# Optimization experiments

Hardware: AMD Instinct MI355X
Metric: run time of the kernel (lower is better)

The kernel has to match this reference:

```python
import jax, jax.numpy as jnp
import numpy as np

# Dims: CrossMambaBlock(dim=256, H=32, W=32); inner Mamba(d_model=512, expand=1,
# d_state=16, bimamba_type='v2', if_devide_out=True, use_norm=True)
B, N, C = 4, 1024, 256
D_MODEL = 2 * C          # 512 (mamba d_model)
D_INNER = D_MODEL        # expand=1
D_STATE = 16
DT_RANK = 32             # ceil(512/16)
D_CONV = 4


def _ln(x, g, b, eps=1e-5):
    m = jnp.mean(x, axis=-1, keepdims=True)
    v = jnp.var(x, axis=-1, keepdims=True)
    return (x - m) * jax.lax.rsqrt(v + eps) * g + b


def _depthwise_causal_conv(x, w, b):
    # x: (B, d, L), w: (d, 1, k) -> causal conv (pad k-1 left), matches Conv1d(padding=k-1)[..., :L]
    y = jax.lax.conv_general_dilated(
        x, w, window_strides=(1,), padding=[(D_CONV - 1, 0)],
        feature_group_count=D_INNER, dimension_numbers=('NCH', 'OIH', 'NCH'))
    return y + b[None, :, None]


def _selective_scan(u, delta, A, Bm, Cm, Dv):
    # u, delta: (B, d, L); A: (d, n); Bm, Cm: (B, n, L); Dv: (d,)
    dA = jnp.exp(jnp.einsum('bdl,dn->lbdn', delta, A))
    dBu = jnp.einsum('bdl,bnl->lbdn', delta * u, Bm)
    Ct = jnp.transpose(Cm, (2, 0, 1))  # (L, B, n)

    def step(h, inp):
        dA_t, dBu_t, c_t = inp
        h = dA_t * h + dBu_t                          # (B, d, n)
        y = jnp.einsum('bdn,bn->bd', h, c_t)
        return h, y

    h0 = jnp.zeros((u.shape[0], u.shape[1], A.shape[1]), u.dtype)
    _, ys = jax.lax.scan(step, h0, (dA, dBu, Ct))
    y = jnp.transpose(ys, (1, 2, 0))                  # (B, d, L)
    return y + Dv[:, None] * u


def _mamba_dir(xz, conv_w, conv_b, xproj_w, dt_w, dt_b, A_log, Dv):
    x, z = jnp.split(xz, 2, axis=1)                   # each (B, d_inner, L)
    x = jax.nn.silu(_depthwise_causal_conv(x, conv_w, conv_b))
    x_dbl = jnp.einsum('bdl,ed->bel', x, xproj_w)     # (B, dt_rank+2n, L)
    dt = x_dbl[:, :DT_RANK]
    Bm = x_dbl[:, DT_RANK:DT_RANK + D_STATE]
    Cm = x_dbl[:, DT_RANK + D_STATE:]
    delta = jax.nn.softplus(jnp.einsum('brl,dr->bdl', dt, dt_w) + dt_b[None, :, None])
    A = -jnp.exp(A_log)
    y = _selective_scan(x, delta, A, Bm, Cm, Dv)
    return y * jax.nn.silu(z)                         # (B, d_inner, L)


def _forward(input0, input1, norm0_g, norm0_b, norm1_g, norm1_b, in_proj_w,
             convf_w, convf_b, convb_w, convb_b, xprojf_w, xprojb_w,
             dtf_w, dtf_b, dtb_w, dtb_b, A_log_f, A_log_b, D_f, D_b,
             mnorm_g, mnorm_b, outproj_w, pnorm_g, pnorm_b,
             projback_w, projback_b, cw_w, cw_b, cwln_g, cwln_b):
    i0 = jnp.nan_to_num(input0, nan=0.0, posinf=1.0, neginf=-1.0)
    i1 = jnp.nan_to_num(input1, nan=0.0, posinf=1.0, neginf=-1.0)
    skip = i0
    x0n = _ln(i0, norm0_g, norm0_b)
    x1n = _ln(i1, norm1_g, norm1_b)
    combined = jnp.concatenate([x0n, x1n], axis=-1)   # (B, N, 2C)
    weight = jax.nn.sigmoid(_ln(combined @ cw_w.T + cw_b, cwln_g, cwln_b))
    weight = jnp.clip(weight, 0.01, 0.99)
    # Mamba (bimamba v2): shared in_proj, two directional scans
    xz = jnp.einsum('bld,ed->bel', combined, in_proj_w)  # (B, 2*d_inner, L)
    out_f = _mamba_dir(xz, convf_w, convf_b, xprojf_w, dtf_w, dtf_b, A_log_f, D_f)
    out_b = _mamba_dir(jnp.flip(xz, -1), convb_w, convb_b, xprojb_w, dtb_w, dtb_b, A_log_b, D_b)
    y = (out_f + jnp.flip(out_b, -1)) * 0.5           # if_devide_out
    y = _ln(jnp.transpose(y, (0, 2, 1)), mnorm_g, mnorm_b)  # use_norm
    out = y @ outproj_w.T                              # (B, N, 2C)
    out = _ln(out, pnorm_g, pnorm_b)
    out = out @ projback_w.T + projback_b              # (B, N, C)
    out = jnp.nan_to_num(out, nan=0.0, posinf=1.0, neginf=-1.0)
    out = out * weight + x0n * (1.0 - weight)
    return out + skip


def setup_inputs() -> dict:
    key = jax.random.key(0)
    ks = iter(jax.random.split(key, 40))
    def rn(shape, s=0.02):
        return jax.random.normal(next(ks), shape, jnp.float32) * s
    inp = {}
    inp['input0'] = jax.random.normal(next(ks), (B, N, C), jnp.float32)
    inp['input1'] = jax.random.normal(next(ks), (B, N, C), jnp.float32)
    for nm in ['norm0', 'norm1']:
        inp[nm + '_g'] = jnp.ones((C,), jnp.float32)
        inp[nm + '_b'] = jnp.zeros((C,), jnp.float32)
    inp['in_proj_w'] = rn((2 * D_INNER, D_MODEL))
    for t in ['f', 'b']:
        inp['conv%s_w' % t] = rn((D_INNER, 1, D_CONV), 0.1)
        inp['conv%s_b' % t] = jnp.zeros((D_INNER,), jnp.float32)
        inp['xproj%s_w' % t] = rn((DT_RANK + 2 * D_STATE, D_INNER))
        inp['dt%s_w' % t] = rn((D_INNER, DT_RANK), 0.05)
        inp['dt%s_b' % t] = rn((D_INNER,), 0.05)
        inp['A_log_%s' % t] = jnp.log(jnp.broadcast_to(
            jnp.arange(1, D_STATE + 1, dtype=jnp.float32), (D_INNER, D_STATE)))
        inp['D_%s' % t] = jnp.ones((D_INNER,), jnp.float32)
    inp['mnorm_g'] = jnp.ones((D_INNER,), jnp.float32)
    inp['mnorm_b'] = jnp.zeros((D_INNER,), jnp.float32)
    inp['outproj_w'] = rn((D_MODEL, D_INNER))
    inp['pnorm_g'] = jnp.ones((D_MODEL,), jnp.float32)
    inp['pnorm_b'] = jnp.zeros((D_MODEL,), jnp.float32)
    inp['projback_w'] = rn((C, D_MODEL))
    inp['projback_b'] = jnp.zeros((C,), jnp.float32)
    inp['cw_w'] = rn((C, D_MODEL))
    inp['cw_b'] = jnp.zeros((C,), jnp.float32)
    inp['cwln_g'] = jnp.ones((C,), jnp.float32)
    inp['cwln_b'] = jnp.zeros((C,), jnp.float32)
    return inp


def reference(input0, input1, norm0_g, norm0_b, norm1_g, norm1_b, in_proj_w,
              convf_w, convf_b, convb_w, convb_b, xprojf_w, xprojb_w,
              dtf_w, dtf_b, dtb_w, dtb_b, A_log_f, A_log_b, D_f, D_b,
              mnorm_g, mnorm_b, outproj_w, pnorm_g, pnorm_b,
              projback_w, projback_b, cw_w, cw_b, cwln_g, cwln_b):
    return _forward(input0, input1, norm0_g, norm0_b, norm1_g, norm1_b, in_proj_w,
                    convf_w, convf_b, convb_w, convb_b, xprojf_w, xprojb_w,
                    dtf_w, dtf_b, dtb_w, dtb_b, A_log_f, A_log_b, D_f, D_b,
                    mnorm_g, mnorm_b, outproj_w, pnorm_g, pnorm_b,
                    projback_w, projback_b, cw_w, cw_b, cwln_g, cwln_b)
```

## Files before the change

### kernel.cpp

```cpp
#include <hip/hip_runtime.h>

#define BDIM 4
#define SEQ 1024
#define CH 256
#define DMODEL 512
#define DINNER 512
#define DSTATE 16
#define DTRANK 32
#define NROWS (BDIM * SEQ)
#define NCHUNK 32
#define CHUNK (SEQ / NCHUNK)

typedef unsigned short ushort_t;

__device__ __forceinline__ float nan2num(float x) {
    if (isnan(x)) return 0.f;
    if (isinf(x)) return x > 0.f ? 1.f : -1.f;
    return x;
}

__device__ __forceinline__ float silu_f(float x) { return x / (1.f + __expf(-x)); }
__device__ __forceinline__ float sigmoid_f(float x) { return 1.f / (1.f + __expf(-x)); }
__device__ __forceinline__ float softplus_f(float x) {
    return x > 20.f ? x : log1pf(__expf(x));
}

__device__ __forceinline__ ushort_t f2bf(float x) {
    union { float f; unsigned u; } v; v.f = x;
    unsigned r = v.u + 0x7fff + ((v.u >> 16) & 1);
    return (ushort_t)(r >> 16);
}
__device__ __forceinline__ float bf2f(ushort_t x) {
    union { unsigned u; float f; } v; v.u = ((unsigned)x) << 16;
    return v.f;
}

using bf16x8 = __attribute__((ext_vector_type(8))) __bf16;
using f32x4  = __attribute__((ext_vector_type(4))) float;

__device__ __forceinline__ void wave_reduce2(float& s, float& q) {
#pragma unroll
    for (int m = 32; m > 0; m >>= 1) {
        s += __shfl_xor(s, m);
        q += __shfl_xor(q, m);
    }
}

#define SZ_INPROJ (1024 * 512)
#define SZ_CW     (256 * 512)
#define SZ_XP     (64 * 512)
#define SZ_DT     (512 * 32)
#define SZ_OUTP   (512 * 512)
#define SZ_PROJB  (256 * 512)
#define SZ_WTOT   (SZ_INPROJ + SZ_CW + 2 * SZ_XP + 2 * SZ_DT + SZ_OUTP + SZ_PROJB)

__global__ __launch_bounds__(256) void convert_weights_kernel(
        const float* __restrict__ w0, const float* __restrict__ w1,
        const float* __restrict__ w2, const float* __restrict__ w3,
        const float* __restrict__ w4, const float* __restrict__ w5,
        const float* __restrict__ w6, const float* __restrict__ w7,
        ushort_t* __restrict__ out) {
    int i = blockIdx.x * 256 + threadIdx.x;
    if (i >= SZ_WTOT) return;
    int j = i;
    const float* src;
    if (j < SZ_INPROJ) { src = w0; }
    else { j -= SZ_INPROJ;
        if (j < SZ_CW) { src = w1; }
        else { j -= SZ_CW;
            if (j < SZ_XP) { src = w2; }
            else { j -= SZ_XP;
                if (j < SZ_XP) { src = w3; }
                else { j -= SZ_XP;
                    if (j < SZ_DT) { src = w4; }
                    else { j -= SZ_DT;
                        if (j < SZ_DT) { src = w5; }
                        else { j -= SZ_DT;
                            if (j < SZ_OUTP) { src = w6; }
                            else { j -= SZ_OUTP; src = w7; }
                        }
                    }
                }
            }
        }
    }
    out[i] = f2bf(src[j]);
}

__global__ __launch_bounds__(256) void ln01_kernel(
        const float* __restrict__ i0, const float* __restrict__ i1,
        const float* __restrict__ g0, const float* __restrict__ b0,
        const float* __restrict__ g1, const float* __restrict__ b1,
        float* __restrict__ x0n, ushort_t* __restrict__ combined) {
    int w = threadIdx.x >> 6, lane = threadIdx.x & 63;
    int row = blockIdx.x * 4 + w;

    float4 v = ((const float4*)(i0 + row * CH))[lane];
    v.x = nan2num(v.x); v.y = nan2num(v.y); v.z = nan2num(v.z); v.w = nan2num(v.w);
    float s = v.x + v.y + v.z + v.w;
    float q = v.x * v.x + v.y * v.y + v.z * v.z + v.w * v.w;
    wave_reduce2(s, q);
    float m = s / (float)CH;
    float r = rsqrtf(q / (float)CH - m * m + 1e-5f);
    float4 g = ((const float4*)g0)[lane];
    float4 bb = ((const float4*)b0)[lane];
    float4 o;
    o.x = (v.x - m) * r * g.x + bb.x;
    o.y = (v.y - m) * r * g.y + bb.y;
    o.z = (v.z - m) * r * g.z + bb.z;
    o.w = (v.w - m) * r * g.w + bb.w;
    ((float4*)(x0n + row * CH))[lane] = o;
    *(ushort4*)(combined + row * DMODEL + lane * 4) =
        make_ushort4(f2bf(o.x), f2bf(o.y), f2bf(o.z), f2bf(o.w));

    v = ((const float4*)(i1 + row * CH))[lane];
    v.x = nan2num(v.x); v.y = nan2num(v.y); v.z = nan2num(v.z); v.w = nan2num(v.w);
    s = v.x + v.y + v.z + v.w;
    q = v.x * v.x + v.y * v.y + v.z * v.z + v.w * v.w;
    wave_reduce2(s, q);
    m = s / (float)CH;
    r = rsqrtf(q / (float)CH - m * m + 1e-5f);
    g = ((const float4*)g1)[lane];
    bb = ((const float4*)b1)[lane];
    o.x = (v.x - m) * r * g.x + bb.x;
    o.y = (v.y - m) * r * g.y + bb.y;
    o.z = (v.z - m) * r * g.z + bb.z;
    o.w = (v.w - m) * r * g.w + bb.w;
    *(ushort4*)(combined + row * DMODEL + CH + lane * 4) =
        make_ushort4(f2bf(o.x), f2bf(o.y), f2bf(o.z), f2bf(o.w));
}

template<int ACT>
__global__ __launch_bounds__(256) void gemm64_kernel(
        const ushort_t* __restrict__ A0, const ushort_t* __restrict__ A1, int lda,
        const ushort_t* __restrict__ W0, const ushort_t* __restrict__ W1, int ldw,
        ushort_t* __restrict__ C0, ushort_t* __restrict__ C1, int ldc,
        int K, const float* __restrict__ bias0, const float* __restrict__ bias1) {
    const ushort_t* A = blockIdx.z ? A1 : A0;
    const ushort_t* W = blockIdx.z ? W1 : W0;
    ushort_t* C = blockIdx.z ? C1 : C0;
    const float* bias = blockIdx.z ? bias1 : bias0;

    __shared__ __align__(16) ushort_t As[64][40];
    __shared__ __align__(16) ushort_t Ws[64][40];
    const int t = threadIdx.x;
    const int m0 = blockIdx.y * 64;
    const int n0 = blockIdx.x * 64;
    const int w = t >> 6;
    const int lane = t & 63;
    const int lane16 = lane & 15;
    const int quad = lane >> 4;
    const int wr = (w >> 1) * 32;
    const int wc = (w & 1) * 32;
    const int srow = t >> 2;
    const int sc8 = (t & 3) * 8;

    f32x4 acc[2][2] = {};

    for (int k0 = 0; k0 < K; k0 += 32) {
        float4 av = *(const float4*)(A + (m0 + srow) * lda + k0 + sc8);
        float4 wv = *(const float4*)(W + (n0 + srow) * ldw + k0 + sc8);
        *(float4*)&As[srow][sc8] = av;
        *(float4*)&Ws[srow][sc8] = wv;
        __syncthreads();

        bf16x8 af[2], bfr[2];
#pragma unroll
        for (int i = 0; i < 2; ++i) {
            af[i]  = *(bf16x8*)&As[wr + i * 16 + lane16][quad * 8];
            bfr[i] = *(bf16x8*)&Ws[wc + i * 16 + lane16][quad * 8];
        }
#pragma unroll
        for (int i = 0; i < 2; ++i)
#pragma unroll
            for (int j = 0; j < 2; ++j)
                acc[i][j] = __builtin_amdgcn_mfma_f32_16x16x32_bf16(af[i], bfr[j], acc[i][j], 0, 0, 0);
        __syncthreads();
    }

#pragma unroll
    for (int j = 0; j < 2; ++j) {
        int col = n0 + wc + j * 16 + lane16;
        float bv = bias ? bias[col] : 0.f;
#pragma unroll
        for (int i = 0; i < 2; ++i) {
#pragma unroll
            for (int r = 0; r < 4; ++r) {
                int row = m0 + wr + i * 16 + quad * 4 + r;
                float c = acc[i][j][r] + bv;
                if (ACT == 1) c = softplus_f(c);
                C[row * ldc + col] = f2bf(c);
            }
        }
    }
}

template<int ACT>
__global__ __launch_bounds__(256) void gemm128_kernel(
        const ushort_t* __restrict__ A0, const ushort_t* __restrict__ A1, int lda,
        const ushort_t* __restrict__ W0, const ushort_t* __restrict__ W1, int ldw,
        ushort_t* __restrict__ C0, ushort_t* __restrict__ C1, int ldc,
        int K, const float* __restrict__ bias0, const float* __restrict__ bias1) {
    const ushort_t* A = blockIdx.z ? A1 : A0;
    const ushort_t* W = blockIdx.z ? W1 : W0;
    ushort_t* C = blockIdx.z ? C1 : C0;
    const float* bias = blockIdx.z ? bias1 : bias0;

    __shared__ __align__(16) ushort_t As[128][40];
    __shared__ __align__(16) ushort_t Ws[64][40];
    const int t = threadIdx.x;
    const int m0 = blockIdx.y * 128;
    const int n0 = blockIdx.x * 64;
    const int w = t >> 6;
    const int lane = t & 63;
    const int lane16 = lane & 15;
    const int quad = lane >> 4;
    const int wr = (w >> 1) * 64;
    const int wc = (w & 1) * 32;
    const int arow = t >> 1;
    const int ac = (t & 1) * 16;
    const int srow = t >> 2;
    const int sc8 = (t & 3) * 8;

    f32x4 acc[4][2] = {};

    for (int k0 = 0; k0 < K; k0 += 32) {
        float4 a0 = *(const float4*)(A + (m0 + arow) * lda + k0 + ac);
        float4 a1 = *(const float4*)(A + (m0 + arow) * lda + k0 + ac + 8);
        float4 wv = *(const float4*)(W + (n0 + srow) * ldw + k0 + sc8);
        *(float4*)&As[arow][ac] = a0;
        *(float4*)&As[arow][ac + 8] = a1;
        *(float4*)&Ws[srow][sc8] = wv;
        __syncthreads();

        bf16x8 af[4], bfr[2];
#pragma unroll
        for (int i = 0; i < 4; ++i)
            af[i] = *(bf16x8*)&As[wr + i * 16 + lane16][quad * 8];
#pragma unroll
        for (int j = 0; j < 2; ++j)
            bfr[j] = *(bf16x8*)&Ws[wc + j * 16 + lane16][quad * 8];
#pragma unroll
        for (int i = 0; i < 4; ++i)
#pragma unroll
            for (int j = 0; j < 2; ++j)
                acc[i][j] = __builtin_amdgcn_mfma_f32_16x16x32_bf16(af[i], bfr[j], acc[i][j], 0, 0, 0);
        __syncthreads();
    }

#pragma unroll
    for (int j = 0; j < 2; ++j) {
        int col = n0 + wc + j * 16 + lane16;
        float bv = bias ? bias[col] : 0.f;
#pragma unroll
        for (int i = 0; i < 4; ++i) {
#pragma unroll
            for (int r = 0; r < 4; ++r) {
                int row = m0 + wr + i * 16 + quad * 4 + r;
                float c = acc[i][j][r] + bv;
                if (ACT == 1) c = softplus_f(c);
                C[row * ldc + col] = f2bf(c);
            }
        }
    }
}

__global__ __launch_bounds__(256) void gemm_projback_final_kernel(
        const ushort_t* __restrict__ A, int lda,
        const ushort_t* __restrict__ W, int ldw,
        int K, const float* __restrict__ bias,
        const ushort_t* __restrict__ wgt, const float* __restrict__ x0n,
        const float* __restrict__ i0, float* __restrict__ out) {
    __shared__ __align__(16) ushort_t As[64][40];
    __shared__ __align__(16) ushort_t Ws[64][40];
    const int t = threadIdx.x;
    const int m0 = blockIdx.y * 64;
    const int n0 = blockIdx.x * 64;
    const int w = t >> 6;
    const int lane = t & 63;
    const int lane16 = lane & 15;
    const int quad = lane >> 4;
    const int wr = (w >> 1) * 32;
    const int wc = (w & 1) * 32;
    const int srow = t >> 2;
    const int sc8 = (t & 3) * 8;

    f32x4 acc[2][2] = {};

    for (int k0 = 0; k0 < K; k0 += 32) {
        float4 av = *(const float4*)(A + (m0 + srow) * lda + k0 + sc8);
        float4 wv = *(const float4*)(W + (n0 + srow) * ldw + k0 + sc8);
        *(float4*)&As[srow][sc8] = av;
        *(float4*)&Ws[srow][sc8] = wv;
        __syncthreads();

        bf16x8 af[2], bfr[2];
#pragma unroll
        for (int i = 0; i < 2; ++i) {
            af[i]  = *(bf16x8*)&As[wr + i * 16 + lane16][quad * 8];
            bfr[i] = *(bf16x8*)&Ws[wc + i * 16 + lane16][quad * 8];
        }
#pragma unroll
        for (int i = 0; i < 2; ++i)
#pragma unroll
            for (int j = 0; j < 2; ++j)
                acc[i][j] = __builtin_amdgcn_mfma_f32_16x16x32_bf16(af[i], bfr[j], acc[i][j], 0, 0, 0);
        __syncthreads();
    }

#pragma unroll
    for (int j = 0; j < 2; ++j) {
        int col = n0 + wc + j * 16 + lane16;
        float bv = bias[col];
#pragma unroll
        for (int i = 0; i < 2; ++i) {
#pragma unroll
            for (int r = 0; r < 4; ++r) {
                int row = m0 + wr + i * 16 + quad * 4 + r;
                float o = nan2num(acc[i][j][r] + bv);
                float wv = bf2f(wgt[row * CH + col]);
                float xv = x0n[row * CH + col];
                float sk = nan2num(i0[row * CH + col]);
                out[row * CH + col] = o * wv + xv * (1.f - wv) + sk;
            }
        }
    }
}

__global__ __launch_bounds__(256) void weight_ln_kernel(
        ushort_t* __restrict__ wbuf, const float* __restrict__ g, const float* __restrict__ b) {
    int w = threadIdx.x >> 6, lane = threadIdx.x & 63;
    int row = blockIdx.x * 4 + w;
    ushort4 raw = *(const ushort4*)(wbuf + row * CH + lane * 4);
    float4 v = make_float4(bf2f(raw.x), bf2f(raw.y), bf2f(raw.z), bf2f(raw.w));
    float s = v.x + v.y + v.z + v.w;
    float q = v.x * v.x + v.y * v.y + v.z * v.z + v.w * v.w;
    wave_reduce2(s, q);
    float m = s / (float)CH;
    float r = rsqrtf(q / (float)CH - m * m + 1e-5f);
    float4 g4 = ((const float4*)g)[lane];
    float4 b4 = ((const float4*)b)[lane];
    float ox = fminf(fmaxf(sigmoid_f((v.x - m) * r * g4.x + b4.x), 0.01f), 0.99f);
    float oy = fminf(fmaxf(sigmoid_f((v.y - m) * r * g4.y + b4.y), 0.01f), 0.99f);
    float oz = fminf(fmaxf(sigmoid_f((v.z - m) * r * g4.z + b4.z), 0.01f), 0.99f);
    float ow = fminf(fmaxf(sigmoid_f((v.w - m) * r * g4.w + b4.w), 0.01f), 0.99f);
    *(ushort4*)(wbuf + row * CH + lane * 4) = make_ushort4(f2bf(ox), f2bf(oy), f2bf(oz), f2bf(ow));
}

__global__ __launch_bounds__(256) void conv_both_kernel(
        const ushort_t* __restrict__ xz,
        const float* __restrict__ wf, const float* __restrict__ wbf,
        const float* __restrict__ wb, const float* __restrict__ wbb,
        ushort_t* __restrict__ outf, ushort_t* __restrict__ outb) {
    int flat = blockIdx.x * 256 + threadIdx.x;
    int d = flat & (DINNER - 1);
    int row = flat >> 9;
    int l = row & (SEQ - 1);
    int b = row >> 10;
    float accf = wbf[d], accb = wbb[d];
#pragma unroll
    for (int k = 0; k < 4; ++k) {
        int jf = l - 3 + k;
        if (jf >= 0) accf += bf2f(xz[(b * SEQ + jf) * (2 * DINNER) + d]) * wf[d * 4 + k];
        int jb = l + 3 - k;
        if (jb < SEQ) accb += bf2f(xz[(b * SEQ + jb) * (2 * DINNER) + d]) * wb[d * 4 + k];
    }
    outf[flat] = f2bf(silu_f(accf));
    outb[(b * SEQ + (SEQ - 1 - l)) * DINNER + d] = f2bf(silu_f(accb));
}

__global__ __launch_bounds__(256) void scan_pass1_kernel(
        const ushort_t* __restrict__ df, const ushort_t* __restrict__ db,
        const ushort_t* __restrict__ uf, const ushort_t* __restrict__ ub,
        const ushort_t* __restrict__ xf, const ushort_t* __restrict__ xb,
        const float* __restrict__ Alf, const float* __restrict__ Alb,
        float* __restrict__ cAf, float* __restrict__ cAb,
        float* __restrict__ cHf, float* __restrict__ cHb) {
    const int dir = blockIdx.z >> 2;
    const int b = blockIdx.z & 3;
    const ushort_t* delta = dir ? db : df;
    const ushort_t* u     = dir ? ub : uf;
    const ushort_t* xdbl  = dir ? xb : xf;
    const float* A_log    = dir ? Alb : Alf;
    float* chunkA = dir ? cAb : cAf;
    float* chunkH = dir ? cHb : cHf;

    const int c = blockIdx.y;
    const int d = blockIdx.x * 256 + threadIdx.x;
    const int base = b * SEQ + c * CHUNK;

    __shared__ float sB[CHUNK][16];
    {
        int t = threadIdx.x;
        if (t < CHUNK * 2) {
            int row = t >> 1, f8 = (t & 1) * 8;
            float4 raw = *(const float4*)(xdbl + (base + row) * 64 + DTRANK + f8);
            const ushort_t* us = (const ushort_t*)&raw;
#pragma unroll
            for (int k = 0; k < 8; ++k) sB[row][f8 + k] = bf2f(us[k]);
        }
    }
    __syncthreads();

    float a[DSTATE];
#pragma unroll
    for (int n = 0; n < DSTATE; n += 4) {
        float4 al = *(const float4*)(A_log + d * DSTATE + n);
        a[n] = -__expf(al.x); a[n + 1] = -__expf(al.y);
        a[n + 2] = -__expf(al.z); a[n + 3] = -__expf(al.w);
    }
    float h[DSTATE];
#pragma unroll
    for (int n = 0; n < DSTATE; ++n) h[n] = 0.f;

    float sumdl = 0.f;
    float dl = bf2f(delta[base * DINNER + d]);
    float ul = bf2f(u[base * DINNER + d]);
    for (int s = 0; s < CHUNK; ++s) {
        int nrow = base + ((s + 1 < CHUNK) ? s + 1 : s);
        float dln = bf2f(delta[nrow * DINNER + d]);
        float uln = bf2f(u[nrow * DINNER + d]);
        float dlul = dl * ul;
        sumdl += dl;
#pragma unroll
        for (int g = 0; g < 4; ++g) {
            float4 B4 = *(const float4*)&sB[s][g * 4];
            float dA0 = __expf(dl * a[g * 4 + 0]);
            float dA1 = __expf(dl * a[g * 4 + 1]);
            float dA2 = __expf(dl * a[g * 4 + 2]);
            float dA3 = __expf(dl * a[g * 4 + 3]);
            h[g * 4 + 0] = dA0 * h[g * 4 + 0] + dlul * B4.x;
            h[g * 4 + 1] = dA1 * h[g * 4 + 1] + dlul * B4.y;
            h[g * 4 + 2] = dA2 * h[g * 4 + 2] + dlul * B4.z;
            h[g * 4 + 3] = dA3 * h[g * 4 + 3] + dlul * B4.w;
        }
        dl = dln; ul = uln;
    }

    int idx = ((b * NCHUNK + c) * DINNER + d) * DSTATE;
#pragma unroll
    for (int n = 0; n < DSTATE; n += 4) {
        float4 P4 = make_float4(__expf(a[n] * sumdl), __expf(a[n + 1] * sumdl),
                                __expf(a[n + 2] * sumdl), __expf(a[n + 3] * sumdl));
        *(float4*)(chunkA + idx + n) = P4;
        *(float4*)(chunkH + idx + n) = make_float4(h[n], h[n + 1], h[n + 2], h[n + 3]);
    }
}

__global__ __launch_bounds__(256) void scan_pass2_kernel(
        const float* __restrict__ cAf, const float* __restrict__ cAb,
        float* __restrict__ cHf, float* __restrict__ cHb) {
    int tid = blockIdx.x * 256 + threadIdx.x;
    int dir = tid >> 15;
    int rr = tid & 32767;
    int b = rr >> 13;
    int rem = rr & 8191;
    const float* chunkA = dir ? cAb : cAf;
    float* chunkH = dir ? cHb : cHf;
    float h = 0.f;
    for (int c = 0; c < NCHUNK; ++c) {
        int idx = (b * NCHUNK + c) * (DINNER * DSTATE) + rem;
        float Ac = chunkA[idx];
        float Hc = chunkH[idx];
        chunkH[idx] = h;
        h = Ac * h + Hc;
    }
}

__global__ __launch_bounds__(256) void scan_pass3_kernel(
        const ushort_t* __restrict__ df, const ushort_t* __restrict__ db,
        const ushort_t* __restrict__ uf, const ushort_t* __restrict__ ub,
        const ushort_t* __restrict__ xf, const ushort_t* __restrict__ xb,
        const float* __restrict__ Alf, const float* __restrict__ Alb,
        const float* __restrict__ Dvf, const float* __restrict__ Dvb,
        const float* __restrict__ hfb, const float* __restrict__ hbb,
        ushort_t* __restrict__ yfo, ushort_t* __restrict__ ybo) {
    const int dir = blockIdx.z >> 2;
    const int b = blockIdx.z & 3;
    const ushort_t* delta = dir ? db : df;
    const ushort_t* u     = dir ? ub : uf;
    const ushort_t* xdbl  = dir ? xb : xf;
    const float* A_log    = dir ? Alb : Alf;
    const float* Dv       = dir ? Dvb : Dvf;
    const float* hin      = dir ? hbb : hfb;
    ushort_t* yout        = dir ? ybo : yfo;

    const int c = blockIdx.y;
    const int d = blockIdx.x * 256 + threadIdx.x;
    const int base = b * SEQ + c * CHUNK;

    __shared__ float sBC[CHUNK][32];
    {
        int t = threadIdx.x;
        if (t < CHUNK * 4) {
            int row = t >> 2, f8 = (t & 3) * 8;
            float4 raw = *(const float4*)(xdbl + (base + row) * 64 + DTRANK + f8);
            const ushort_t* us = (const ushort_t*)&raw;
#pragma unroll
            for (int k = 0; k < 8; ++k) sBC[row][f8 + k] = bf2f(us[k]);
        }
    }
    __syncthreads();

    float a[DSTATE];
#pragma unroll
    for (int n = 0; n < DSTATE; n += 4) {
        float4 al = *(const float4*)(A_log + d * DSTATE + n);
        a[n] = -__expf(al.x); a[n + 1] = -__expf(al.y);
        a[n + 2] = -__expf(al.z); a[n + 3] = -__expf(al.w);
    }
    float h[DSTATE];
    {
        int idx = ((b * NCHUNK + c) * DINNER + d) * DSTATE;
#pragma unroll
        for (int n = 0; n < DSTATE; n += 4) {
            float4 h4 = *(const float4*)(hin + idx + n);
            h[n] = h4.x; h[n + 1] = h4.y; h[n + 2] = h4.z; h[n + 3] = h4.w;
        }
    }
    const float Dd = Dv[d];

    float dl = bf2f(delta[base * DINNER + d]);
    float ul = bf2f(u[base * DINNER + d]);
    for (int s = 0; s < CHUNK; ++s) {
        int nrow = base + ((s + 1 < CHUNK) ? s + 1 : s);
        float dln = bf2f(delta[nrow * DINNER + d]);
        float uln = bf2f(u[nrow * DINNER + d]);
        float dlul = dl * ul;
        float y = 0.f;
#pragma unroll
        for (int g = 0; g < 4; ++g) {
            float4 B4 = *(const float4*)&sBC[s][g * 4];
            float4 C4 = *(const float4*)&sBC[s][16 + g * 4];
            float dA0 = __expf(dl * a[g * 4 + 0]);
            float dA1 = __expf(dl * a[g * 4 + 1]);
            float dA2 = __expf(dl * a[g * 4 + 2]);
            float dA3 = __expf(dl * a[g * 4 + 3]);
            h[g * 4 + 0] = dA0 * h[g * 4 + 0] + dlul * B4.x;
            h[g * 4 + 1] = dA1 * h[g * 4 + 1] + dlul * B4.y;
            h[g * 4 + 2] = dA2 * h[g * 4 + 2] + dlul * B4.z;
            h[g * 4 + 3] = dA3 * h[g * 4 + 3] + dlul * B4.w;
            y += h[g * 4 + 0] * C4.x + h[g * 4 + 1] * C4.y
               + h[g * 4 + 2] * C4.z + h[g * 4 + 3] * C4.w;
        }
        int lpos = c * CHUNK + s;
        int orow = b * SEQ + (dir ? (SEQ - 1 - lpos) : lpos);
        yout[orow * DINNER + d] = f2bf(y + Dd * ul);
        dl = dln; ul = uln;
    }
}

__global__ __launch_bounds__(256) void combine_mnorm_kernel(
        const ushort_t* __restrict__ yf, const ushort_t* __restrict__ yb,
        const ushort_t* __restrict__ xz,
        const float* __restrict__ g, const float* __restrict__ b,
        ushort_t* __restrict__ yn) {
    int w = threadIdx.x >> 6, lane = threadIdx.x & 63;
    int row = blockIdx.x * 4 + w;
    float4 rf = *(const float4*)(yf + row * DINNER + lane * 8);
    float4 rb = *(const float4*)(yb + row * DINNER + lane * 8);
    float4 rz = *(const float4*)(xz + row * (2 * DINNER) + DINNER + lane * 8);
    const ushort_t* uf = (const ushort_t*)&rf;
    const ushort_t* ub = (const ushort_t*)&rb;
    const ushort_t* uz = (const ushort_t*)&rz;
    float v[8];
    float s = 0.f, q = 0.f;
#pragma unroll
    for (int k = 0; k < 8; ++k) {
        float val = 0.5f * (bf2f(uf[k]) + bf2f(ub[k])) * silu_f(bf2f(uz[k]));
        v[k] = val; s += val; q += val * val;
    }
    wave_reduce2(s, q);
    float m = s / (float)DINNER;
    float r = rsqrtf(q / (float)DINNER - m * m + 1e-5f);
    ushort_t o[8];
#pragma unroll
    for (int k = 0; k < 8; ++k)
        o[k] = f2bf((v[k] - m) * r * g[lane * 8 + k] + b[lane * 8 + k]);
    *(ushort4*)(yn + row * DINNER + lane * 8) = make_ushort4(o[0], o[1], o[2], o[3]);
    *(ushort4*)(yn + row * DINNER + lane * 8 + 4) = make_ushort4(o[4], o[5], o[6], o[7]);
}

__global__ __launch_bounds__(256) void ln512_kernel(
        const ushort_t* __restrict__ in,
        const float* __restrict__ g, const float* __restrict__ b,
        ushort_t* __restrict__ out) {
    int w = threadIdx.x >> 6, lane = threadIdx.x & 63;
    int row = blockIdx.x * 4 + w;
    float4 raw = *(const float4*)(in + row * DMODEL + lane * 8);
    const ushort_t* us = (const ushort_t*)&raw;
    float v[8];
    float s = 0.f, q = 0.f;
#pragma unroll
    for (int k = 0; k < 8; ++k) {
        v[k] = bf2f(us[k]); s += v[k]; q += v[k] * v[k];
    }
    wave_reduce2(s, q);
    float m = s / (float)DMODEL;
    float r = rsqrtf(q / (float)DMODEL - m * m + 1e-5f);
    ushort_t o[8];
#pragma unroll
    for (int k = 0; k < 8; ++k)
        o[k] = f2bf((v[k] - m) * r * g[lane * 8 + k] + b[lane * 8 + k]);
    *(ushort4*)(out + row * DMODEL + lane * 8) = make_ushort4(o[0], o[1], o[2], o[3]);
    *(ushort4*)(out + row * DMODEL + lane * 8 + 4) = make_ushort4(o[4], o[5], o[6], o[7]);
}

extern "C" void kernel_launch(void* const* d_in, const int* in_sizes, int n_in,
                              void* d_out, int out_size, void* d_ws, size_t ws_size,
                              hipStream_t stream) {
    (void)in_sizes; (void)n_in; (void)out_size; (void)ws_size;
    const float* input0    = (const float*)d_in[0];
    const float* input1    = (const float*)d_in[1];
    const float* norm0_g   = (const float*)d_in[2];
    const float* norm0_b   = (const float*)d_in[3];
    const float* norm1_g   = (const float*)d_in[4];
    const float* norm1_b   = (const float*)d_in[5];
    const float* in_proj_w = (const float*)d_in[6];
    const float* convf_w   = (const float*)d_in[7];
    const float* convf_b   = (const float*)d_in[8];
    const float* xprojf_w  = (const float*)d_in[9];
    const float* dtf_w     = (const float*)d_in[10];
    const float* dtf_b     = (const float*)d_in[11];
    const float* A_log_f   = (const float*)d_in[12];
    const float* D_f       = (const float*)d_in[13];
    const float* convb_w   = (const float*)d_in[14];
    const float* convb_b   = (const float*)d_in[15];
    const float* xprojb_w  = (const float*)d_in[16];
    const float* dtb_w     = (const float*)d_in[17];
    const float* dtb_b     = (const float*)d_in[18];
    const float* A_log_b   = (const float*)d_in[19];
    const float* D_b       = (const float*)d_in[20];
    const float* mnorm_g   = (const float*)d_in[21];
    const float* mnorm_b   = (const float*)d_in[22];
    const float* outproj_w = (const float*)d_in[23];
    const float* pnorm_g   = (const float*)d_in[24];
    const float* pnorm_b   = (const float*)d_in[25];
    const float* projback_w= (const float*)d_in[26];
    const float* projback_b= (const float*)d_in[27];
    const float* cw_w      = (const float*)d_in[28];
    const float* cw_b      = (const float*)d_in[29];
    const float* cwln_g    = (const float*)d_in[30];
    const float* cwln_b    = (const float*)d_in[31];

    float* wsf = (float*)d_ws;
    float* x0n      = wsf;
    float* chunkA_f = x0n + 1048576;
    float* chunkA_b = chunkA_f + 1048576;
    float* chunkH_f = chunkA_b + 1048576;
    float* chunkH_b = chunkH_f + 1048576;
    ushort_t* wsu = (ushort_t*)(chunkH_b + 1048576);
    ushort_t* combined = wsu;
    ushort_t* xz       = combined + 2097152;
    ushort_t* weight   = xz + 4194304;
    ushort_t* xdbl_f   = weight + 1048576;
    ushort_t* xdbl_b   = xdbl_f + 262144;
    ushort_t* xconv_f  = xdbl_b + 262144;
    ushort_t* xconv_b  = xconv_f + 2097152;
    ushort_t* delta_f  = xconv_b + 2097152;
    ushort_t* delta_b  = delta_f + 2097152;
    ushort_t* y_f      = delta_b + 2097152;
    ushort_t* y_b      = y_f + 2097152;
    ushort_t* yn       = y_b + 2097152;
    ushort_t* o1       = yn + 2097152;
    ushort_t* on1      = o1 + 2097152;
    ushort_t* wb       = on1 + 2097152;
    ushort_t* w_inproj = wb;
    ushort_t* w_cw     = w_inproj + SZ_INPROJ;
    ushort_t* w_xpf    = w_cw + SZ_CW;
    ushort_t* w_xpb    = w_xpf + SZ_XP;
    ushort_t* w_dtf    = w_xpb + SZ_XP;
    ushort_t* w_dtb    = w_dtf + SZ_DT;
    ushort_t* w_outp   = w_dtb + SZ_DT;
    ushort_t* w_projb  = w_outp + SZ_OUTP;

    convert_weights_kernel<<<(SZ_WTOT + 255) / 256, 256, 0, stream>>>(
        in_proj_w, cw_w, xprojf_w, xprojb_w, dtf_w, dtb_w, outproj_w, projback_w, wb);

    ln01_kernel<<<NROWS / 4, 256, 0, stream>>>(input0, input1, norm0_g, norm0_b,
                                               norm1_g, norm1_b, x0n, combined);

    gemm128_kernel<0><<<dim3(16, 32, 1), 256, 0, stream>>>(
        combined, combined, DMODEL, w_inproj, w_inproj, DMODEL,
        xz, xz, 2 * DINNER, DMODEL, nullptr, nullptr);

    gemm64_kernel<0><<<dim3(4, 64, 1), 256, 0, stream>>>(
        combined, combined, DMODEL, w_cw, w_cw, DMODEL,
        weight, weight, CH, DMODEL, cw_b, cw_b);

    weight_ln_kernel<<<NROWS / 4, 256, 0, stream>>>(weight, cwln_g, cwln_b);

    conv_both_kernel<<<NROWS * DINNER / 256, 256, 0, stream>>>(
        xz, convf_w, convf_b, convb_w, convb_b, xconv_f, xconv_b);

    gemm64_kernel<0><<<dim3(1, 64, 2), 256, 0, stream>>>(
        xconv_f, xconv_b, DINNER, w_xpf, w_xpb, DINNER,
        xdbl_f, xdbl_b, 64, DINNER, nullptr, nullptr);

    gemm128_kernel<1><<<dim3(8, 32, 2), 256, 0, stream>>>(
        xdbl_f, xdbl_b, 64, w_dtf, w_dtb, DTRANK,
        delta_f, delta_b, DINNER, DTRANK, dtf_b, dtb_b);

    dim3 sgrid(DINNER / 256, NCHUNK, 2 * BDIM);
    scan_pass1_kernel<<<sgrid, 256, 0, stream>>>(
        delta_f, delta_b, xconv_f, xconv_b, xdbl_f, xdbl_b, A_log_f, A_log_b,
        chunkA_f, chunkA_b, chunkH_f, chunkH_b);
    scan_pass2_kernel<<<256, 256, 0, stream>>>(chunkA_f, chunkA_b, chunkH_f, chunkH_b);
    scan_pass3_kernel<<<sgrid, 256, 0, stream>>>(
        delta_f, delta_b, xconv_f, xconv_b, xdbl_f, xdbl_b, A_log_f, A_log_b,
        D_f, D_b, chunkH_f, chunkH_b, y_f, y_b);

    combine_mnorm_kernel<<<NROWS / 4, 256, 0, stream>>>(y_f, y_b, xz, mnorm_g, mnorm_b, yn);

    gemm128_kernel<0><<<dim3(8, 32, 1), 256, 0, stream>>>(
        yn, yn, DINNER, w_outp, w_outp, DINNER,
        o1, o1, DMODEL, DINNER, nullptr, nullptr);

    ln512_kernel<<<NROWS / 4, 256, 0, stream>>>(o1, pnorm_g, pnorm_b, on1);

    gemm_projback_final_kernel<<<dim3(4, 64, 1), 256, 0, stream>>>(
        on1, DMODEL, w_projb, DMODEL, DMODEL, projback_b,
        weight, x0n, input0, (float*)d_out);
}
```

Before: 276.5 us.

## Fuse scan output pass with gate and norm, vectorize conv, use more chunks

The final scan pass now handles both directions for a chunk in one 512-thread block. It pairs forward chunk c with the matching reversed backward chunk, so it can average the two outputs, apply the SiLU(z) gate and the per-row LayerNorm in registers and shared memory. This removes the separate combine_mnorm kernel and the y_f/y_b intermediate buffers. The depthwise conv kernel is rewritten so each thread processes 8 channels with 16-byte vector loads and stores, reusing a 7-row window for both directions. The chunk count doubles to 64 for more scan parallelism, which costs larger chunk-state buffers and more work in the cross-chunk pass. The register prefetch in pass1 is also dropped.

```diff
diff --git a/kernel.cpp b/kernel.cpp
--- a/kernel.cpp
+++ b/kernel.cpp
@@ -8,7 +8,7 @@
 #define DSTATE 16
 #define DTRANK 32
 #define NROWS (BDIM * SEQ)
-#define NCHUNK 32
+#define NCHUNK 64
 #define CHUNK (SEQ / NCHUNK)
 
 typedef unsigned short ushort_t;
@@ -352,21 +352,58 @@
         const float* __restrict__ wf, const float* __restrict__ wbf,
         const float* __restrict__ wb, const float* __restrict__ wbb,
         ushort_t* __restrict__ outf, ushort_t* __restrict__ outb) {
-    int flat = blockIdx.x * 256 + threadIdx.x;
-    int d = flat & (DINNER - 1);
-    int row = flat >> 9;
-    int l = row & (SEQ - 1);
-    int b = row >> 10;
-    float accf = wbf[d], accb = wbb[d];
-#pragma unroll
-    for (int k = 0; k < 4; ++k) {
-        int jf = l - 3 + k;
-        if (jf >= 0) accf += bf2f(xz[(b * SEQ + jf) * (2 * DINNER) + d]) * wf[d * 4 + k];
-        int jb = l + 3 - k;
-        if (jb < SEQ) accb += bf2f(xz[(b * SEQ + jb) * (2 * DINNER) + d]) * wb[d * 4 + k];
-    }
-    outf[flat] = f2bf(silu_f(accf));
-    outb[(b * SEQ + (SEQ - 1 - l)) * DINNER + d] = f2bf(silu_f(accb));
+    const int t = threadIdx.x;
+    const int lane = t & 63;
+    const int row = blockIdx.x * 4 + (t >> 6);
+    const int l = row & (SEQ - 1);
+    const int b = row >> 10;
+    const int d0 = lane * 8;
+
+    float x[7][8];
+#pragma unroll
+    for (int j = 0; j < 7; ++j) {
+        int ll = l - 3 + j;
+        if (ll >= 0 && ll < SEQ) {
+            float4 raw = *(const float4*)(xz + (b * SEQ + ll) * (2 * DINNER) + d0);
+            const ushort_t* us = (const ushort_t*)&raw;
+#pragma unroll
+            for (int k = 0; k < 8; ++k) x[j][k] = bf2f(us[k]);
+        } else {
+#pragma unroll
+            for (int k = 0; k < 8; ++k) x[j][k] = 0.f;
+        }
+    }
+
+    float wfv[32], wbv[32];
+#pragma unroll
+    for (int q = 0; q < 8; ++q) {
+        float4 a = *(const float4*)(wf + d0 * 4 + q * 4);
+        wfv[q * 4] = a.x; wfv[q * 4 + 1] = a.y; wfv[q * 4 + 2] = a.z; wfv[q * 4 + 3] = a.w;
+        float4 c = *(const float4*)(wb + d0 * 4 + q * 4);
+        wbv[q * 4] = c.x; wbv[q * 4 + 1] = c.y; wbv[q * 4 + 2] = c.z; wbv[q * 4 + 3] = c.w;
+    }
+    float4 bf0 = *(const float4*)(wbf + d0), bf1 = *(const float4*)(wbf + d0 + 4);
+    float4 bb0 = *(const float4*)(wbb + d0), bb1 = *(const float4*)(wbb + d0 + 4);
+    float biasf[8] = {bf0.x, bf0.y, bf0.z, bf0.w, bf1.x, bf1.y, bf1.z, bf1.w};
+    float biasb[8] = {bb0.x, bb0.y, bb0.z, bb0.w, bb1.x, bb1.y, bb1.z, bb1.w};
+
+    ushort_t of[8], ob[8];
+#pragma unroll
+    for (int q = 0; q < 8; ++q) {
+        float accf = biasf[q], accb = biasb[q];
+#pragma unroll
+        for (int k = 0; k < 4; ++k) {
+            accf += x[k][q] * wfv[q * 4 + k];
+            accb += x[6 - k][q] * wbv[q * 4 + k];
+        }
+        of[q] = f2bf(silu_f(accf));
+        ob[q] = f2bf(silu_f(accb));
+    }
+    *(ushort4*)(outf + row * DINNER + d0)     = make_ushort4(of[0], of[1], of[2], of[3]);
+    *(ushort4*)(outf + row * DINNER + d0 + 4) = make_ushort4(of[4], of[5], of[6], of[7]);
+    ushort_t* pb = outb + (b * SEQ + (SEQ - 1 - l)) * DINNER + d0;
+    *(ushort4*)pb       = make_ushort4(ob[0], ob[1], ob[2], ob[3]);
+    *(ushort4*)(pb + 4) = make_ushort4(ob[4], ob[5], ob[6], ob[7]);
 }
 
 __global__ __launch_bounds__(256) void scan_pass1_kernel(
@@ -414,12 +451,10 @@
     for (int n = 0; n < DSTATE; ++n) h[n] = 0.f;
 
     float sumdl = 0.f;
-    float dl = bf2f(delta[base * DINNER + d]);
-    float ul = bf2f(u[base * DINNER + d]);
     for (int s = 0; s < CHUNK; ++s) {
-        int nrow = base + ((s + 1 < CHUNK) ? s + 1 : s);
-        float dln = bf2f(delta[nrow * DINNER + d]);
-        float uln = bf2f(u[nrow * DINNER + d]);
+        int row = base + s;
+        float dl = bf2f(delta[row * DINNER + d]);
+        float ul = bf2f(u[row * DINNER + d]);
         float dlul = dl * ul;
         sumdl += dl;
 #pragma unroll
@@ -434,7 +469,6 @@
             h[g * 4 + 2] = dA2 * h[g * 4 + 2] + dlul * B4.z;
             h[g * 4 + 3] = dA3 * h[g * 4 + 3] + dlul * B4.w;
         }
-        dl = dln; ul = uln;
     }
 
     int idx = ((b * NCHUNK + c) * DINNER + d) * DSTATE;
@@ -467,118 +501,143 @@
     }
 }
 
-__global__ __launch_bounds__(256) void scan_pass3_kernel(
+__global__ __launch_bounds__(512) void scan_pass3_fused_kernel(
         const ushort_t* __restrict__ df, const ushort_t* __restrict__ db,
         const ushort_t* __restrict__ uf, const ushort_t* __restrict__ ub,
         const ushort_t* __restrict__ xf, const ushort_t* __restrict__ xb,
         const float* __restrict__ Alf, const float* __restrict__ Alb,
         const float* __restrict__ Dvf, const float* __restrict__ Dvb,
         const float* __restrict__ hfb, const float* __restrict__ hbb,
-        ushort_t* __restrict__ yfo, ushort_t* __restrict__ ybo) {
-    const int dir = blockIdx.z >> 2;
-    const int b = blockIdx.z & 3;
-    const ushort_t* delta = dir ? db : df;
-    const ushort_t* u     = dir ? ub : uf;
-    const ushort_t* xdbl  = dir ? xb : xf;
-    const float* A_log    = dir ? Alb : Alf;
-    const float* Dv       = dir ? Dvb : Dvf;
-    const float* hin      = dir ? hbb : hfb;
-    ushort_t* yout        = dir ? ybo : yfo;
-
-    const int c = blockIdx.y;
-    const int d = blockIdx.x * 256 + threadIdx.x;
-    const int base = b * SEQ + c * CHUNK;
-
-    __shared__ float sBC[CHUNK][32];
+        const ushort_t* __restrict__ xz,
+        const float* __restrict__ mg, const float* __restrict__ mb,
+        ushort_t* __restrict__ yn) {
+    const int d = threadIdx.x;
+    const int c = blockIdx.x;
+    const int b = blockIdx.y;
+    const int c2 = NCHUNK - 1 - c;
+    const int base_f = b * SEQ + c * CHUNK;
+    const int base_b = b * SEQ + c2 * CHUNK;
+
+    __shared__ float sBC[2][CHUNK][32];
+    __shared__ float sP[CHUNK][8], sQ[CHUNK][8], sM[CHUNK], sR[CHUNK];
     {
         int t = threadIdx.x;
-        if (t < CHUNK * 4) {
-            int row = t >> 2, f8 = (t & 3) * 8;
-            float4 raw = *(const float4*)(xdbl + (base + row) * 64 + DTRANK + f8);
+        if (t < 128) {
+            int dir = t >> 6;
+            int rr = (t >> 2) & 15;
+            int f8 = (t & 3) * 8;
+            const ushort_t* xd = dir ? xb : xf;
+            int bs = dir ? base_b : base_f;
+            float4 raw = *(const float4*)(xd + (bs + rr) * 64 + DTRANK + f8);
             const ushort_t* us = (const ushort_t*)&raw;
 #pragma unroll
-            for (int k = 0; k < 8; ++k) sBC[row][f8 + k] = bf2f(us[k]);
+            for (int k = 0; k < 8; ++k) sBC[dir][rr][f8 + k] = bf2f(us[k]);
         }
     }
     __syncthreads();
 
-    float a[DSTATE];
-#pragma unroll
-    for (int n = 0; n < DSTATE; n += 4) {
-        float4 al = *(const float4*)(A_log + d * DSTATE + n);
-        a[n] = -__expf(al.x); a[n + 1] = -__expf(al.y);
-        a[n + 2] = -__expf(al.z); a[n + 3] = -__expf(al.w);
-    }
-    float h[DSTATE];
+    float yv[CHUNK];
+
     {
-        int idx = ((b * NCHUNK + c) * DINNER + d) * DSTATE;
+        float a[DSTATE], h[DSTATE];
 #pragma unroll
         for (int n = 0; n < DSTATE; n += 4) {
-            float4 h4 = *(const float4*)(hin + idx + n);
+            float4 al = *(const float4*)(Alf + d * DSTATE + n);
+            a[n] = -__expf(al.x); a[n + 1] = -__expf(al.y);
+            a[n + 2] = -__expf(al.z); a[n + 3] = -__expf(al.w);
+            float4 h4 = *(const float4*)(hfb + ((b * NCHUNK + c) * DINNER + d) * DSTATE + n);
             h[n] = h4.x; h[n + 1] = h4.y; h[n + 2] = h4.z; h[n + 3] = h4.w;
         }
-    }
-    const float Dd = Dv[d];
-
-    float dl = bf2f(delta[base * DINNER + d]);
-    float ul = bf2f(u[base * DINNER + d]);
+        float Dd = Dvf[d];
+        for (int s = 0; s < CHUNK; ++s) {
+            int row = base_f + s;
+            float dl = bf2f(df[row * DINNER + d]);
+            float ul = bf2f(uf[row * DINNER + d]);
+            float dlul = dl * ul;
+            float y = 0.f;
+#pragma unroll
+            for (int g = 0; g < 4; ++g) {
+                float4 B4 = *(const float4*)&sBC[0][s][g * 4];
+                float4 C4 = *(const float4*)&sBC[0][s][16 + g * 4];
+                float dA0 = __expf(dl * a[g * 4 + 0]);
+                float dA1 = __expf(dl * a[g * 4 + 1]);
+                float dA2 = __expf(dl * a[g * 4 + 2]);
+                float dA3 = __expf(dl * a[g * 4 + 3]);
+                h[g * 4 + 0] = dA0 * h[g * 4 + 0] + dlul * B4.x;
+                h[g * 4 + 1] = dA1 * h[g * 4 + 1] + dlul * B4.y;
+                h[g * 4 + 2] = dA2 * h[g * 4 + 2] + dlul * B4.z;
+                h[g * 4 + 3] = dA3 * h[g * 4 + 3] + dlul * B4.w;
+                y += h[g * 4 + 0] * C4.x + h[g * 4 + 1] * C4.y
+                   + h[g * 4 + 2] * C4.z + h[g * 4 + 3] * C4.w;
+            }
+            yv[s] = y + Dd * ul;
+        }
+    }
+
+    {
+        float a[DSTATE], h[DSTATE];
+#pragma unroll
+        for (int n = 0; n < DSTATE; n += 4) {
+            float4 al = *(const float4*)(Alb + d * DSTATE + n);
+            a[n] = -__expf(al.x); a[n + 1] = -__expf(al.y);
+            a[n + 2] = -__expf(al.z); a[n + 3] = -__expf(al.w);
+            float4 h4 = *(const float4*)(hbb + ((b * NCHUNK + c2) * DINNER + d) * DSTATE + n);
+            h[n] = h4.x; h[n + 1] = h4.y; h[n + 2] = h4.z; h[n + 3] = h4.w;
+        }
+        float Dd = Dvb[d];
+        for (int s = 0; s < CHUNK; ++s) {
+            int row = base_b + s;
+            float dl = bf2f(db[row * DINNER + d]);
+            float ul = bf2f(ub[row * DINNER + d]);
+            float dlul = dl * ul;
+            float y = 0.f;
+#pragma unroll
+            for (int g = 0; g < 4; ++g) {
+                float4 B4 = *(const float4*)&sBC[1][s][g * 4];
+                float4 C4 = *(const float4*)&sBC[1][s][16 + g * 4];
+                float dA0 = __expf(dl * a[g * 4 + 0]);
+                float dA1 = __expf(dl * a[g * 4 + 1]);
+                float dA2 = __expf(dl * a[g * 4 + 2]);
+                float dA3 = __expf(dl * a[g * 4 + 3]);
+                h[g * 4 + 0] = dA0 * h[g * 4 + 0] + dlul * B4.x;
+                h[g * 4 + 1] = dA1 * h[g * 4 + 1] + dlul * B4.y;
+                h[g * 4 + 2] = dA2 * h[g * 4 + 2] + dlul * B4.z;
+                h[g * 4 + 3] = dA3 * h[g * 4 + 3] + dlul * B4.w;
+                y += h[g * 4 + 0] * C4.x + h[g * 4 + 1] * C4.y
+                   + h[g * 4 + 2] * C4.z + h[g * 4 + 3] * C4.w;
+            }
+            yv[CHUNK - 1 - s] += y + Dd * ul;
+        }
+    }
+
+    const int w = threadIdx.x >> 6, lane = threadIdx.x & 63;
+    float v[CHUNK];
+#pragma unroll
     for (int s = 0; s < CHUNK; ++s) {
-        int nrow = base + ((s + 1 < CHUNK) ? s + 1 : s);
-        float dln = bf2f(delta[nrow * DINNER + d]);
-        float uln = bf2f(u[nrow * DINNER + d]);
-        float dlul = dl * ul;
-        float y = 0.f;
-#pragma unroll
-        for (int g = 0; g < 4; ++g) {
-            float4 B4 = *(const float4*)&sBC[s][g * 4];
-            float4 C4 = *(const float4*)&sBC[s][16 + g * 4];
-            float dA0 = __expf(dl * a[g * 4 + 0]);
-            float dA1 = __expf(dl * a[g * 4 + 1]);
-            float dA2 = __expf(dl * a[g * 4 + 2]);
-            float dA3 = __expf(dl * a[g * 4 + 3]);
-            h[g * 4 + 0] = dA0 * h[g * 4 + 0] + dlul * B4.x;
-            h[g * 4 + 1] = dA1 * h[g * 4 + 1] + dlul * B4.y;
-            h[g * 4 + 2] = dA2 * h[g * 4 + 2] + dlul * B4.z;
-            h[g * 4 + 3] = dA3 * h[g * 4 + 3] + dlul * B4.w;
-            y += h[g * 4 + 0] * C4.x + h[g * 4 + 1] * C4.y
-               + h[g * 4 + 2] * C4.z + h[g * 4 + 3] * C4.w;
-        }
-        int lpos = c * CHUNK + s;
-        int orow = b * SEQ + (dir ? (SEQ - 1 - lpos) : lpos);
-        yout[orow * DINNER + d] = f2bf(y + Dd * ul);
-        dl = dln; ul = uln;
-    }
-}
-
-__global__ __launch_bounds__(256) void combine_mnorm_kernel(
-        const ushort_t* __restrict__ yf, const ushort_t* __restrict__ yb,
-        const ushort_t* __restrict__ xz,
-        const float* __restrict__ g, const float* __restrict__ b,
-        ushort_t* __restrict__ yn) {
-    int w = threadIdx.x >> 6, lane = threadIdx.x & 63;
-    int row = blockIdx.x * 4 + w;
-    float4 rf = *(const float4*)(yf + row * DINNER + lane * 8);
-    float4 rb = *(const float4*)(yb + row * DINNER + lane * 8);
-    float4 rz = *(const float4*)(xz + row * (2 * DINNER) + DINNER + lane * 8);
-    const ushort_t* uf = (const ushort_t*)&rf;
-    const ushort_t* ub = (const ushort_t*)&rb;
-    const ushort_t* uz = (const ushort_t*)&rz;
-    float v[8];
-    float s = 0.f, q = 0.f;
-#pragma unroll
-    for (int k = 0; k < 8; ++k) {
-        float val = 0.5f * (bf2f(uf[k]) + bf2f(ub[k])) * silu_f(bf2f(uz[k]));
-        v[k] = val; s += val; q += val * val;
-    }
-    wave_reduce2(s, q);
-    float m = s / (float)DINNER;
-    float r = rsqrtf(q / (float)DINNER - m * m + 1e-5f);
-    ushort_t o[8];
-#pragma unroll
-    for (int k = 0; k < 8; ++k)
-        o[k] = f2bf((v[k] - m) * r * g[lane * 8 + k] + b[lane * 8 + k]);
-    *(ushort4*)(yn + row * DINNER + lane * 8) = make_ushort4(o[0], o[1], o[2], o[3]);
-    *(ushort4*)(yn + row * DINNER + lane * 8 + 4) = make_ushort4(o[4], o[5], o[6], o[7]);
+        float z = bf2f(xz[(base_f + s) * (2 * DINNER) + DINNER + d]);
+        v[s] = 0.5f * yv[s] * silu_f(z);
+    }
+#pragma unroll
+    for (int s = 0; s < CHUNK; ++s) {
+        float ss = v[s], qq = v[s] * v[s];
+        wave_reduce2(ss, qq);
+        if (lane == 0) { sP[s][w] = ss; sQ[s][w] = qq; }
+    }
+    __syncthreads();
+    if (threadIdx.x < CHUNK) {
+        int s = threadIdx.x;
+        float ss = 0.f, qq = 0.f;
+#pragma unroll
+        for (int w2 = 0; w2 < 8; ++w2) { ss += sP[s][w2]; qq += sQ[s][w2]; }
+        float m = ss / (float)DINNER;
+        sM[s] = m;
+        sR[s] = rsqrtf(qq / (float)DINNER - m * m + 1e-5f);
+    }
+    __syncthreads();
+    float gd = mg[d], bd = mb[d];
+#pragma unroll
+    for (int s = 0; s < CHUNK; ++s)
+        yn[(base_f + s) * DINNER + d] = f2bf((v[s] - sM[s]) * sR[s] * gd + bd);
 }
 
 __global__ __launch_bounds__(256) void ln512_kernel(
@@ -646,10 +705,10 @@
     float* wsf = (float*)d_ws;
     float* x0n      = wsf;
     float* chunkA_f = x0n + 1048576;
-    float* chunkA_b = chunkA_f + 1048576;
-    float* chunkH_f = chunkA_b + 1048576;
-    float* chunkH_b = chunkH_f + 1048576;
-    ushort_t* wsu = (ushort_t*)(chunkH_b + 1048576);
+    float* chunkA_b = chunkA_f + 2097152;
+    float* chunkH_f = chunkA_b + 2097152;
+    float* chunkH_b = chunkH_f + 2097152;
+    ushort_t* wsu = (ushort_t*)(chunkH_b + 2097152);
     ushort_t* combined = wsu;
     ushort_t* xz       = combined + 2097152;
     ushort_t* weight   = xz + 4194304;
@@ -659,9 +718,7 @@
     ushort_t* xconv_b  = xconv_f + 2097152;
     ushort_t* delta_f  = xconv_b + 2097152;
     ushort_t* delta_b  = delta_f + 2097152;
-    ushort_t* y_f      = delta_b + 2097152;
-    ushort_t* y_b      = y_f + 2097152;
-    ushort_t* yn       = y_b + 2097152;
+    ushort_t* yn       = delta_b + 2097152;
     ushort_t* o1       = yn + 2097152;
     ushort_t* on1      = o1 + 2097152;
     ushort_t* wb       = on1 + 2097152;
@@ -690,7 +747,7 @@
 
     weight_ln_kernel<<<NROWS / 4, 256, 0, stream>>>(weight, cwln_g, cwln_b);
 
-    conv_both_kernel<<<NROWS * DINNER / 256, 256, 0, stream>>>(
+    conv_both_kernel<<<NROWS / 4, 256, 0, stream>>>(
         xz, convf_w, convf_b, convb_w, convb_b, xconv_f, xconv_b);
 
     gemm64_kernel<0><<<dim3(1, 64, 2), 256, 0, stream>>>(
@@ -701,16 +758,13 @@
         xdbl_f, xdbl_b, 64, w_dtf, w_dtb, DTRANK,
         delta_f, delta_b, DINNER, DTRANK, dtf_b, dtb_b);
 
-    dim3 sgrid(DINNER / 256, NCHUNK, 2 * BDIM);
-    scan_pass1_kernel<<<sgrid, 256, 0, stream>>>(
+    scan_pass1_kernel<<<dim3(DINNER / 256, NCHUNK, 2 * BDIM), 256, 0, stream>>>(
         delta_f, delta_b, xconv_f, xconv_b, xdbl_f, xdbl_b, A_log_f, A_log_b,
         chunkA_f, chunkA_b, chunkH_f, chunkH_b);
     scan_pass2_kernel<<<256, 256, 0, stream>>>(chunkA_f, chunkA_b, chunkH_f, chunkH_b);
-    scan_pass3_kernel<<<sgrid, 256, 0, stream>>>(
+    scan_pass3_fused_kernel<<<dim3(NCHUNK, BDIM), 512, 0, stream>>>(
         delta_f, delta_b, xconv_f, xconv_b, xdbl_f, xdbl_b, A_log_f, A_log_b,
-        D_f, D_b, chunkH_f, chunkH_b, y_f, y_b);
-
-    combine_mnorm_kernel<<<NROWS / 4, 256, 0, stream>>>(y_f, y_b, xz, mnorm_g, mnorm_b, yn);
+        D_f, D_b, chunkH_f, chunkH_b, xz, mnorm_g, mnorm_b, yn);
 
     gemm128_kernel<0><<<dim3(8, 32, 1), 256, 0, stream>>>(
         yn, yn, DINNER, w_outp, w_outp, DINNER,
```

After: 628.2 us. 127% more time.
